# Optimization experiments

Hardware: AMD Instinct MI355X
Metric: run time of the kernel (lower is better)

The kernel has to match this reference:

```python
import jax, jax.numpy as jnp
import numpy as np

HEADS = 8

def _ln(x, g, b):
    m = jnp.mean(x, -1, keepdims=True)
    v = jnp.var(x, -1, keepdims=True)
    return (x - m) * jax.lax.rsqrt(v + 1e-5) * g + b

def _mha(q, kv, W, b, key_valid):
    # W: [4,E,E] (q,k,v,out proj), b: [4,E]; key_valid: [Sk] bool mask over kv positions
    B, Sq, E = q.shape
    Sk = kv.shape[1]
    D = E // HEADS
    qh = (q @ W[0] + b[0]).reshape(B, Sq, HEADS, D)
    kh = (kv @ W[1] + b[1]).reshape(B, Sk, HEADS, D)
    vh = (kv @ W[2] + b[2]).reshape(B, Sk, HEADS, D)
    s = jnp.einsum('bqhd,bkhd->bhqk', qh, kh) / jnp.sqrt(jnp.asarray(D, q.dtype))
    s = jnp.where(key_valid[None, None, None, :], s, jnp.asarray(-1e9, q.dtype))
    o = jnp.einsum('bhqk,bkhd->bqhd', jax.nn.softmax(s, -1), vh).reshape(B, Sq, E)
    return o @ W[3] + b[3]

def _posenc(S, E):
    pos = np.arange(S)[:, None].astype(np.float32)
    i = np.arange(0, E, 2).astype(np.float32)[None, :]
    ang = pos / np.power(10000.0, i / E)
    pe = np.zeros((S, E), np.float32)
    pe[:, 0::2] = np.sin(ang)
    pe[:, 1::2] = np.cos(ang)
    return jnp.asarray(pe)

def _forward(noise, seeds, inemb_W, inemb_b, g_attn_W, g_attn_b, g_cross_W, g_cross_b,
             g_ffn_W1, g_ffn_b1, g_ffn_W2, g_ffn_b2, g_ln_g, g_ln_b,
             o_attn_W, o_attn_b, o_ffn_W1, o_ffn_b1, o_ffn_W2, o_ffn_b2, o_ln_g, o_ln_b,
             w2v, soft_W, soft_b):
    B, S, E = noise.shape
    V = soft_W.shape[1]
    # inEmb: M stacked linear layers (no activation)
    w = noise
    for i in range(inemb_W.shape[0]):
        w = w @ inemb_W[i] + inemb_b[i]
    pe = _posenc(S, E)[None]  # [1,S,E]
    nB = g_attn_W.shape[0]
    nO = o_attn_W.shape[0]

    def step(carry, t):
        Ybuf, out_sent = carry
        valid = jnp.arange(S) <= t  # grown-sequence mask (no KV cache in original)
        x = Ybuf + pe
        for i in range(nB):  # generator: outTrans decoder blocks (self + cross-attn to w)
            x = _ln(x + _mha(x, x, g_attn_W[i], g_attn_b[i], valid), g_ln_g[i, 0], g_ln_b[i, 0])
            x = _ln(x + _mha(x, w, g_cross_W[i], g_cross_b[i], valid), g_ln_g[i, 1], g_ln_b[i, 1])
            f = jax.nn.relu(x @ g_ffn_W1[i] + g_ffn_b1[i]) @ g_ffn_W2[i] + g_ffn_b2[i]
            x = _ln(x + f, g_ln_g[i, 2], g_ln_b[i, 2])
        for j in range(nO):  # outEmb: inTrans encoder blocks
            x = _ln(x + _mha(x, x, o_attn_W[j], o_attn_b[j], valid), o_ln_g[j, 0], o_ln_b[j, 0])
            f = jax.nn.relu(x @ o_ffn_W1[j] + o_ffn_b1[j]) @ o_ffn_W2[j] + o_ffn_b2[j]
            x = _ln(x + f, o_ln_g[j, 1], o_ln_b[j, 1])
        tok = x[:, t]  # [B,E]
        probs = jax.nn.softmax(tok @ soft_W + soft_b, axis=-1)  # [B,V]
        out_sent = jax.lax.dynamic_update_slice(out_sent, probs[:, None, :], (0, t, 0))
        emb = w2v[jnp.argmax(probs, axis=-1)]  # Word2Vec(one_hot(argmax)) == row lookup
        Ybuf = jax.lax.dynamic_update_slice(Ybuf, emb[:, None, :], (0, t, 0))
        return (Ybuf, out_sent), None

    init = (seeds, jnp.zeros((B, S, V), noise.dtype))
    (_, out_sent), _ = jax.lax.scan(step, init, jnp.arange(S))
    return out_sent

def setup_inputs():
    key = jax.random.key(0)
    ks = jax.random.split(key, 12)
    B, S, E, H, V = 32, 32, 512, 2048, 30000
    M, NB, NO = 2, 2, 1
    def rn(k, shape, s=0.02):
        return jax.random.normal(k, shape, jnp.float32) * s
    return {
        'noise': jax.random.normal(ks[0], (B, S, E), jnp.float32),
        'seeds': jax.random.normal(ks[1], (B, S, E), jnp.float32),
        'inemb_W': rn(ks[2], (M, E, E)), 'inemb_b': jnp.zeros((M, E), jnp.float32),
        'g_attn_W': rn(ks[3], (NB, 4, E, E)), 'g_attn_b': jnp.zeros((NB, 4, E), jnp.float32),
        'g_cross_W': rn(ks[4], (NB, 4, E, E)), 'g_cross_b': jnp.zeros((NB, 4, E), jnp.float32),
        'g_ffn_W1': rn(ks[5], (NB, E, H)), 'g_ffn_b1': jnp.zeros((NB, H), jnp.float32),
        'g_ffn_W2': rn(ks[6], (NB, H, E)), 'g_ffn_b2': jnp.zeros((NB, E), jnp.float32),
        'g_ln_g': jnp.ones((NB, 3, E), jnp.float32), 'g_ln_b': jnp.zeros((NB, 3, E), jnp.float32),
        'o_attn_W': rn(ks[7], (NO, 4, E, E)), 'o_attn_b': jnp.zeros((NO, 4, E), jnp.float32),
        'o_ffn_W1': rn(ks[8], (NO, E, H)), 'o_ffn_b1': jnp.zeros((NO, H), jnp.float32),
        'o_ffn_W2': rn(ks[9], (NO, H, E)), 'o_ffn_b2': jnp.zeros((NO, E), jnp.float32),
        'o_ln_g': jnp.ones((NO, 2, E), jnp.float32), 'o_ln_b': jnp.zeros((NO, 2, E), jnp.float32),
        'w2v': rn(ks[10], (V, E)),
        'soft_W': rn(ks[11], (E, V)), 'soft_b': jnp.zeros((V,), jnp.float32),
    }

def reference(noise, seeds, inemb_W, inemb_b, g_attn_W, g_attn_b, g_cross_W, g_cross_b,
              g_ffn_W1, g_ffn_b1, g_ffn_W2, g_ffn_b2, g_ln_g, g_ln_b,
              o_attn_W, o_attn_b, o_ffn_W1, o_ffn_b1, o_ffn_W2, o_ffn_b2, o_ln_g, o_ln_b,
              w2v, soft_W, soft_b):
    return _forward(noise, seeds, inemb_W, inemb_b, g_attn_W, g_attn_b, g_cross_W, g_cross_b,
                    g_ffn_W1, g_ffn_b1, g_ffn_W2, g_ffn_b2, g_ln_g, g_ln_b,
                    o_attn_W, o_attn_b, o_ffn_W1, o_ffn_b1, o_ffn_W2, o_ffn_b2, o_ln_g, o_ln_b,
                    w2v, soft_W, soft_b)
```

## Files before the change

### kernel.cpp

```cpp
#include <hip/hip_runtime.h>
#include <math.h>

#define E 512
#define S_MAX 32
#define BATCH 32
#define HEADS 8
#define DH 64
#define HID 2048
#define VOCAB 30000

typedef unsigned short u16;
typedef __attribute__((ext_vector_type(8))) short short8;
typedef __attribute__((ext_vector_type(4))) float f32x4;

__device__ __forceinline__ u16 f2bf(float x) {
    union { float f; unsigned u; } v; v.f = x;
    unsigned r = v.u + 0x7fffu + ((v.u >> 16) & 1u);
    return (u16)(r >> 16);
}
__device__ __forceinline__ float bf2f(u16 h) {
    union { unsigned u; float f; } v; v.u = ((unsigned)h) << 16;
    return v.f;
}
__device__ __forceinline__ void split3(float x, u16& h, u16& m, u16& l) {
    h = f2bf(x); float hf = bf2f(h);
    float r1 = x - hf;
    m = f2bf(r1); float mf = bf2f(m);
    l = f2bf(r1 - mf);
}

__global__ void pe_kernel(float* __restrict__ PEp) {
    int s = blockIdx.x;
    for (int e = threadIdx.x; e < E; e += 256) {
        float expo = (float)(e & ~1) / (float)E;
        float den = powf(10000.0f, expo);
        float ang = (float)s / den;
        PEp[s * E + e] = (e & 1) ? cosf(ang) : sinf(ang);
    }
}

__global__ void build_x_kernel(float* __restrict__ X, const float* __restrict__ Ybuf,
                               const float* __restrict__ PEp, int Seff,
                               u16* __restrict__ Xh, u16* __restrict__ Xm, u16* __restrict__ Xl) {
    long idx = (long)blockIdx.x * 256 + threadIdx.x;
    long total = (long)BATCH * Seff * E;
    if (idx >= total) return;
    int e = (int)(idx & (E - 1));
    long mm = idx >> 9;
    int b = (int)(mm / Seff);
    int s = (int)(mm - (long)b * Seff);
    float v = Ybuf[((long)b * S_MAX + s) * E + e] + PEp[s * E + e];
    X[idx] = v;
    u16 h, m, l; split3(v, h, m, l);
    Xh[idx] = h; Xm[idx] = m; Xl[idx] = l;
}

__global__ void split_act_kernel(const float* __restrict__ in, long n,
                                 u16* __restrict__ Ph, u16* __restrict__ Pm, u16* __restrict__ Pl) {
    long i = ((long)blockIdx.x * 256 + threadIdx.x) * 4;
    if (i >= n) return;
    float4 v = *(const float4*)(in + i);
    u16 h, m, l;
    split3(v.x, h, m, l); Ph[i] = h; Pm[i] = m; Pl[i] = l;
    split3(v.y, h, m, l); Ph[i+1] = h; Pm[i+1] = m; Pl[i+1] = l;
    split3(v.z, h, m, l); Ph[i+2] = h; Pm[i+2] = m; Pl[i+2] = l;
    split3(v.w, h, m, l); Ph[i+3] = h; Pm[i+3] = m; Pl[i+3] = l;
}

__global__ __launch_bounds__(256) void wsplit_kernel(const float* __restrict__ W,
                                                     u16* __restrict__ Ph, u16* __restrict__ Pm,
                                                     u16* __restrict__ Pl,
                                                     int K, int N, long wzin, long wzout) {
    int z = blockIdx.z;
    W += (long)z * wzin; Ph += (long)z * wzout; Pm += (long)z * wzout; Pl += (long)z * wzout;
    int n0 = blockIdx.x * 32, k0 = blockIdx.y * 32;
    __shared__ float T[32][33];
    int tid = threadIdx.x;
    int kk = tid >> 3, nn = (tid & 7) * 4;
    float4 v = *(const float4*)&W[(long)(k0 + kk) * N + n0 + nn];
    T[kk][nn + 0] = v.x; T[kk][nn + 1] = v.y; T[kk][nn + 2] = v.z; T[kk][nn + 3] = v.w;
    __syncthreads();
    int n = tid >> 3, k4 = (tid & 7) * 4;
    u16 h[4], m[4], l[4];
#pragma unroll
    for (int j = 0; j < 4; j++) split3(T[k4 + j][n], h[j], m[j], l[j]);
    long o = (long)(n0 + n) * K + k0 + k4;
    *(ushort4*)&Ph[o] = make_ushort4(h[0], h[1], h[2], h[3]);
    *(ushort4*)&Pm[o] = make_ushort4(m[0], m[1], m[2], m[3]);
    *(ushort4*)&Pl[o] = make_ushort4(l[0], l[1], l[2], l[3]);
}

template <int RELU, int WF32, int WSPLIT>
__global__ __launch_bounds__(256) void gemm_mfma(
    const u16* __restrict__ Ah, const u16* __restrict__ Am, const u16* __restrict__ Al,
    const u16* __restrict__ Wh, const u16* __restrict__ Wm, const u16* __restrict__ Wl,
    const float* __restrict__ bias,
    float* __restrict__ C, u16* __restrict__ Ch, u16* __restrict__ Cm, u16* __restrict__ Cl,
    int M, int N, int K, long wz, long cz, long bz) {
    int z = blockIdx.z;
    const u16* Ap[3] = {Ah, Am, Al};
    const u16* Bp[3] = {Wh + (long)z * wz, Wm + (long)z * wz, Wl + (long)z * wz};
    bias += (long)z * bz;
    C += (long)z * cz;
    Ch += (long)z * cz; Cm += (long)z * cz; Cl += (long)z * cz;

    int n0 = blockIdx.x * 64, m0 = blockIdx.y * 64;
    int tid = threadIdx.x, lane = tid & 63, wid = tid >> 6;
    int wr = wid >> 1, wc = wid & 1;

    __shared__ u16 As[3][2048];
    __shared__ u16 Bs[3][2048];

    int srow = (tid >> 6) * 16 + (tid & 15);
    int scol = ((tid >> 4) & 3) * 8;
    int arow = m0 + srow; if (arow >= M) arow = M - 1;
    int brow = n0 + srow;
    long abase = (long)arow * K + scol;
    long bbase = (long)brow * K + scol;

    uint4 ra[3], rb[3];
#pragma unroll
    for (int p = 0; p < 3; p++) {
        ra[p] = *(const uint4*)(Ap[p] + abase);
        rb[p] = *(const uint4*)(Bp[p] + bbase);
    }

    f32x4 acc[2][2];
#pragma unroll
    for (int mi = 0; mi < 2; mi++)
#pragma unroll
        for (int ni = 0; ni < 2; ni++) acc[mi][ni] = (f32x4){0.f, 0.f, 0.f, 0.f};

    int fro = (lane >> 4) * 128 + (lane & 15) * 8;
    const int PA[6] = {0, 0, 1, 1, 0, 2};
    const int PB[6] = {0, 1, 0, 1, 2, 0};

    for (int k0 = 0; k0 < K; k0 += 32) {
#pragma unroll
        for (int p = 0; p < 3; p++) {
            *(uint4*)&As[p][tid * 8] = ra[p];
            *(uint4*)&Bs[p][tid * 8] = rb[p];
        }
        __syncthreads();
        if (k0 + 32 < K) {
#pragma unroll
            for (int p = 0; p < 3; p++) {
                ra[p] = *(const uint4*)(Ap[p] + abase + k0 + 32);
                rb[p] = *(const uint4*)(Bp[p] + bbase + k0 + 32);
            }
        }
        short8 af[3][2], bf[3][2];
#pragma unroll
        for (int p = 0; p < 3; p++) {
#pragma unroll
            for (int q = 0; q < 2; q++) {
                af[p][q] = *(const short8*)&As[p][(wr * 2 + q) * 512 + fro];
                bf[p][q] = *(const short8*)&Bs[p][(wc * 2 + q) * 512 + fro];
            }
        }
#pragma unroll
        for (int u = 0; u < 6; u++) {
#pragma unroll
            for (int mi = 0; mi < 2; mi++)
#pragma unroll
                for (int ni = 0; ni < 2; ni++)
                    acc[mi][ni] = __builtin_amdgcn_mfma_f32_16x16x32_bf16(
                        af[PA[u]][mi], bf[PB[u]][ni], acc[mi][ni], 0, 0, 0);
        }
        __syncthreads();
    }

#pragma unroll
    for (int mi = 0; mi < 2; mi++) {
#pragma unroll
        for (int ni = 0; ni < 2; ni++) {
            int col = n0 + wc * 32 + ni * 16 + (lane & 15);
            float bv = bias[col];
#pragma unroll
            for (int j = 0; j < 4; j++) {
                int row = m0 + wr * 32 + mi * 16 + (lane >> 4) * 4 + j;
                if (row < M) {
                    float v = acc[mi][ni][j] + bv;
                    if (RELU) v = fmaxf(v, 0.f);
                    long idx = (long)row * N + col;
                    if (WF32) C[idx] = v;
                    if (WSPLIT) {
                        u16 hh, mm, ll; split3(v, hh, mm, ll);
                        Ch[idx] = hh; Cm[idx] = mm; Cl[idx] = ll;
                    }
                }
            }
        }
    }
}

__global__ __launch_bounds__(64) void attn_kernel(const float* __restrict__ Q,
                                                  const float* __restrict__ Kp,
                                                  const float* __restrict__ Vp,
                                                  u16* __restrict__ Oh, u16* __restrict__ Om,
                                                  u16* __restrict__ Ol,
                                                  int Seff, int kvBatchStride) {
    int s = blockIdx.x, h = blockIdx.y, b = blockIdx.z;
    int lane = threadIdx.x;
    __shared__ float qs[DH];
    qs[lane] = Q[((long)(b * Seff + s)) * E + h * DH + lane];
    __syncthreads();

    float sc = -INFINITY;
    if (lane < Seff) {
        const float4* k4 = (const float4*)(Kp + (long)b * kvBatchStride + (long)lane * E + h * DH);
        const float4* q4 = (const float4*)qs;
        float acc = 0.f;
#pragma unroll
        for (int d = 0; d < DH / 4; d++) {
            float4 kv = k4[d];
            float4 qv = q4[d];
            acc += qv.x * kv.x; acc += qv.y * kv.y; acc += qv.z * kv.z; acc += qv.w * kv.w;
        }
        sc = acc * 0.125f;
    }
    float m = sc;
#pragma unroll
    for (int off = 32; off; off >>= 1) m = fmaxf(m, __shfl_xor(m, off));
    float p = (lane < Seff) ? expf(sc - m) : 0.f;
    float sum = p;
#pragma unroll
    for (int off = 32; off; off >>= 1) sum += __shfl_xor(sum, off);
    p = p / sum;

    float acc = 0.f;
    const float* vbase = Vp + (long)b * kvBatchStride + h * DH + lane;
    for (int k = 0; k < Seff; k++) {
        float pk = __shfl(p, k);
        acc = fmaf(pk, vbase[(long)k * E], acc);
    }
    long o = ((long)(b * Seff + s)) * E + h * DH + lane;
    u16 hh, mm, ll; split3(acc, hh, mm, ll);
    Oh[o] = hh; Om[o] = mm; Ol[o] = ll;
}

__global__ __launch_bounds__(64) void resid_ln_kernel(float* __restrict__ X,
                                                      const float* __restrict__ Dlt,
                                                      const float* __restrict__ g,
                                                      const float* __restrict__ bb,
                                                      u16* __restrict__ Xh, u16* __restrict__ Xm,
                                                      u16* __restrict__ Xl) {
    long row = blockIdx.x;
    int lane = threadIdx.x;
    float* xr = X + row * E;
    const float* dr = Dlt + row * E;
    float v[8];
    float s = 0.f;
#pragma unroll
    for (int i = 0; i < 8; i++) {
        int e = lane + i * 64;
        v[i] = xr[e] + dr[e];
        s += v[i];
    }
#pragma unroll
    for (int off = 32; off; off >>= 1) s += __shfl_xor(s, off);
    float mean = s * (1.0f / E);
    float sq = 0.f;
#pragma unroll
    for (int i = 0; i < 8; i++) {
        float d = v[i] - mean;
        sq += d * d;
    }
#pragma unroll
    for (int off = 32; off; off >>= 1) sq += __shfl_xor(sq, off);
    float var = sq * (1.0f / E);
    float r = 1.0f / sqrtf(var + 1e-5f);
#pragma unroll
    for (int i = 0; i < 8; i++) {
        int e = lane + i * 64;
        float o = (v[i] - mean) * r * g[e] + bb[e];
        xr[e] = o;
        u16 hh, mm, ll; split3(o, hh, mm, ll);
        long idx = row * E + e;
        Xh[idx] = hh; Xm[idx] = mm; Xl[idx] = ll;
    }
}

__global__ __launch_bounds__(256) void logits_kernel(const float* __restrict__ X,
                                                     const float* __restrict__ SW,
                                                     const float* __restrict__ sb,
                                                     float* __restrict__ Lg,
                                                     int Seff, int t) {
    int nl = threadIdx.x & 63;
    int kq = threadIdx.x >> 6;
    int n = blockIdx.x * 64 + nl;
    bool nok = n < VOCAB;
    float acc[BATCH];
#pragma unroll
    for (int b = 0; b < BATCH; b++) acc[b] = 0.f;
    if (nok) {
        int k0 = kq * 128;
        for (int k = k0; k < k0 + 128; k++) {
            float wv = SW[(long)k * VOCAB + n];
#pragma unroll
            for (int b = 0; b < BATCH; b++) {
                acc[b] = fmaf(X[((long)(b * Seff + t)) * E + k], wv, acc[b]);
            }
        }
    }
    __shared__ float red[4][64];
    for (int b = 0; b < BATCH; b++) {
        red[kq][nl] = acc[b];
        __syncthreads();
        if (kq == 0 && nok) {
            float sum = red[0][nl] + red[1][nl] + red[2][nl] + red[3][nl] + sb[n];
            Lg[(long)b * VOCAB + n] = sum;
        }
        __syncthreads();
    }
}

__global__ __launch_bounds__(256) void softmax_out_kernel(const float* __restrict__ Lg,
                                                          float* __restrict__ Out,
                                                          const float* __restrict__ w2v,
                                                          float* __restrict__ Ybuf, int t) {
    int b = blockIdx.x;
    int tid = threadIdx.x;
    const float* lb = Lg + (long)b * VOCAB;
    __shared__ float red[256];

    float m = -INFINITY;
    for (int n = tid; n < VOCAB; n += 256) m = fmaxf(m, lb[n]);
    red[tid] = m;
    __syncthreads();
    for (int off = 128; off; off >>= 1) {
        if (tid < off) red[tid] = fmaxf(red[tid], red[tid + off]);
        __syncthreads();
    }
    m = red[0];
    __syncthreads();

    float s = 0.f;
    for (int n = tid; n < VOCAB; n += 256) s += expf(lb[n] - m);
    red[tid] = s;
    __syncthreads();
    for (int off = 128; off; off >>= 1) {
        if (tid < off) red[tid] += red[tid + off];
        __syncthreads();
    }
    s = red[0];
    __syncthreads();

    float bestv = -1.0f;
    int besti = VOCAB;
    float* ob = Out + ((long)b * S_MAX + t) * VOCAB;
    for (int n = tid; n < VOCAB; n += 256) {
        float p = expf(lb[n] - m) / s;
        ob[n] = p;
        if (p > bestv) { bestv = p; besti = n; }
    }
    __shared__ float rv[256];
    __shared__ int ri[256];
    rv[tid] = bestv;
    ri[tid] = besti;
    __syncthreads();
    for (int off = 128; off; off >>= 1) {
        if (tid < off) {
            float v2 = rv[tid + off];
            int i2 = ri[tid + off];
            if (v2 > rv[tid] || (v2 == rv[tid] && i2 < ri[tid])) { rv[tid] = v2; ri[tid] = i2; }
        }
        __syncthreads();
    }
    int idx = ri[0];
    float* yb = Ybuf + ((long)b * S_MAX + t) * E;
    for (int e = tid; e < E; e += 256) yb[e] = w2v[(long)idx * E + e];
}

extern "C" void kernel_launch(void* const* d_in, const int* in_sizes, int n_in,
                              void* d_out, int out_size, void* d_ws, size_t ws_size,
                              hipStream_t stream) {
    const float* noise    = (const float*)d_in[0];
    const float* seeds    = (const float*)d_in[1];
    const float* inemb_W  = (const float*)d_in[2];
    const float* inemb_b  = (const float*)d_in[3];
    const float* g_attn_W = (const float*)d_in[4];
    const float* g_attn_b = (const float*)d_in[5];
    const float* g_cross_W= (const float*)d_in[6];
    const float* g_cross_b= (const float*)d_in[7];
    const float* g_ffn_W1 = (const float*)d_in[8];
    const float* g_ffn_b1 = (const float*)d_in[9];
    const float* g_ffn_W2 = (const float*)d_in[10];
    const float* g_ffn_b2 = (const float*)d_in[11];
    const float* g_ln_g   = (const float*)d_in[12];
    const float* g_ln_b   = (const float*)d_in[13];
    const float* o_attn_W = (const float*)d_in[14];
    const float* o_attn_b = (const float*)d_in[15];
    const float* o_ffn_W1 = (const float*)d_in[16];
    const float* o_ffn_b1 = (const float*)d_in[17];
    const float* o_ffn_W2 = (const float*)d_in[18];
    const float* o_ffn_b2 = (const float*)d_in[19];
    const float* o_ln_g   = (const float*)d_in[20];
    const float* o_ln_b   = (const float*)d_in[21];
    const float* w2v      = (const float*)d_in[22];
    const float* soft_W   = (const float*)d_in[23];
    const float* soft_b   = (const float*)d_in[24];
    float* out = (float*)d_out;
    float* ws = (float*)d_ws;

    const long EE  = (long)E * E;
    const long EH  = (long)E * HID;
    const long BSE = (long)BATCH * S_MAX * E;
    const long BSH = (long)BATCH * S_MAX * HID;
    const long WTOT = 46 * EE;

    long off = 0;
    float* PE   = ws + off; off += 16384;
    float* YBUF = ws + off; off += BSE;
    float* X    = ws + off; off += BSE;
    float* TMP  = ws + off; off += BSE;
    float* QKV  = ws + off; off += 3 * BSE;
    float* KWVW = ws + off; off += 4 * BSE;
    float* LG   = ws + off; off += 960000;
    u16* XsH = (u16*)(ws + off); off += 3 * BSE / 2;
    u16* XsM = XsH + BSE; u16* XsL = XsM + BSE;
    u16* AOH = (u16*)(ws + off); off += 3 * BSE / 2;
    u16* AOM = AOH + BSE; u16* AOL = AOM + BSE;
    u16* HBH = (u16*)(ws + off); off += 3 * BSH / 2;
    u16* HBM2 = HBH + BSH; u16* HBL = HBM2 + BSH;
    long baseWords = off;

    bool full = ws_size >= (size_t)(baseWords + 3 * WTOT / 2) * 4;
    long WT_ELEMS = full ? WTOT : 4 * EE;
    u16* WT_H = (u16*)(ws + baseWords);
    u16* WT_M = WT_H + WT_ELEMS;
    u16* WT_L = WT_M + WT_ELEMS;

    const long OFF_INEMB = 0;
    const long OFF_GATTN = 2 * EE;
    const long OFF_GCROSS = 10 * EE;
    const long OFF_OATTN = 18 * EE;
    const long OFF_GF1 = 22 * EE;
    const long OFF_GF2 = 30 * EE;
    const long OFF_OF1 = 38 * EE;
    const long OFF_OF2 = 42 * EE;

    auto WSPL = [&](const float* Wsrc, long offFull, int K, int N, int z) -> long {
        if (full) return offFull;
        wsplit_kernel<<<dim3(N / 32, K / 32, z), dim3(256), 0, stream>>>(
            Wsrc, WT_H, WT_M, WT_L, K, N, (long)K * N, (long)K * N);
        return 0;
    };

    auto GEMM = [&](const u16* Ah, const u16* Am, const u16* Al, long woff,
                    const float* bias, float* C, u16* Ch, u16* Cm, u16* Cl,
                    int M, int N, int K, int Z, long wz, long cz, long bz, int mode) {
        dim3 g(N / 64, (M + 63) / 64, Z);
        const u16* Wh = WT_H + woff; const u16* Wm = WT_M + woff; const u16* Wl = WT_L + woff;
        if (mode == 0)
            gemm_mfma<0, 1, 0><<<g, dim3(256), 0, stream>>>(Ah, Am, Al, Wh, Wm, Wl, bias,
                                                            C, Ch, Cm, Cl, M, N, K, wz, cz, bz);
        else if (mode == 1)
            gemm_mfma<0, 0, 1><<<g, dim3(256), 0, stream>>>(Ah, Am, Al, Wh, Wm, Wl, bias,
                                                            C, Ch, Cm, Cl, M, N, K, wz, cz, bz);
        else
            gemm_mfma<1, 0, 1><<<g, dim3(256), 0, stream>>>(Ah, Am, Al, Wh, Wm, Wl, bias,
                                                            C, Ch, Cm, Cl, M, N, K, wz, cz, bz);
    };

    pe_kernel<<<dim3(S_MAX), dim3(256), 0, stream>>>(PE);
    hipMemcpyAsync(YBUF, seeds, BSE * sizeof(float), hipMemcpyDeviceToDevice, stream);

    if (full) {
        wsplit_kernel<<<dim3(16, 16, 2), dim3(256), 0, stream>>>(inemb_W, WT_H + OFF_INEMB, WT_M + OFF_INEMB, WT_L + OFF_INEMB, 512, 512, EE, EE);
        wsplit_kernel<<<dim3(16, 16, 8), dim3(256), 0, stream>>>(g_attn_W, WT_H + OFF_GATTN, WT_M + OFF_GATTN, WT_L + OFF_GATTN, 512, 512, EE, EE);
        wsplit_kernel<<<dim3(16, 16, 8), dim3(256), 0, stream>>>(g_cross_W, WT_H + OFF_GCROSS, WT_M + OFF_GCROSS, WT_L + OFF_GCROSS, 512, 512, EE, EE);
        wsplit_kernel<<<dim3(16, 16, 4), dim3(256), 0, stream>>>(o_attn_W, WT_H + OFF_OATTN, WT_M + OFF_OATTN, WT_L + OFF_OATTN, 512, 512, EE, EE);
        wsplit_kernel<<<dim3(64, 16, 2), dim3(256), 0, stream>>>(g_ffn_W1, WT_H + OFF_GF1, WT_M + OFF_GF1, WT_L + OFF_GF1, 512, 2048, EH, EH);
        wsplit_kernel<<<dim3(16, 64, 2), dim3(256), 0, stream>>>(g_ffn_W2, WT_H + OFF_GF2, WT_M + OFF_GF2, WT_L + OFF_GF2, 2048, 512, EH, EH);
        wsplit_kernel<<<dim3(64, 16, 1), dim3(256), 0, stream>>>(o_ffn_W1, WT_H + OFF_OF1, WT_M + OFF_OF1, WT_L + OFF_OF1, 512, 2048, EH, EH);
        wsplit_kernel<<<dim3(16, 64, 1), dim3(256), 0, stream>>>(o_ffn_W2, WT_H + OFF_OF2, WT_M + OFF_OF2, WT_L + OFF_OF2, 2048, 512, EH, EH);
    }

    split_act_kernel<<<dim3((int)(BSE / 1024)), dim3(256), 0, stream>>>(noise, BSE, HBH, HBM2, HBL);

    {
        long w = WSPL(inemb_W, OFF_INEMB, 512, 512, 1);
        GEMM(HBH, HBM2, HBL, w, inemb_b, TMP, AOH, AOM, AOL, BATCH * S_MAX, E, E, 1, 0, 0, 0, 1);
        w = WSPL(inemb_W + EE, OFF_INEMB + EE, 512, 512, 1);
        GEMM(AOH, AOM, AOL, w, inemb_b + E, TMP, XsH, XsM, XsL, BATCH * S_MAX, E, E, 1, 0, 0, 0, 1);
    }
    for (int i = 0; i < 2; i++) {
        long w = WSPL(g_cross_W + (i * 4 + 1) * EE, OFF_GCROSS + (i * 4 + 1) * EE, 512, 512, 2);
        GEMM(XsH, XsM, XsL, w, g_cross_b + (i * 4 + 1) * E, KWVW + i * 2 * BSE, AOH, AOM, AOL,
             BATCH * S_MAX, E, E, 2, EE, BSE, E, 0);
    }

    for (int t = 0; t < S_MAX; t++) {
        int Seff = t + 1;
        int Mrows = BATCH * Seff;
        long ME = (long)Mrows * E;
        int total = Mrows * E;

        build_x_kernel<<<dim3((total + 255) / 256), dim3(256), 0, stream>>>(X, YBUF, PE, Seff,
                                                                            XsH, XsM, XsL);

        for (int i = 0; i < 2; i++) {
            long w = WSPL(g_attn_W + (long)i * 4 * EE, OFF_GATTN + i * 4 * EE, 512, 512, 3);
            GEMM(XsH, XsM, XsL, w, g_attn_b + (long)i * 4 * E, QKV, AOH, AOM, AOL,
                 Mrows, E, E, 3, EE, ME, E, 0);
            attn_kernel<<<dim3(Seff, HEADS, BATCH), dim3(64), 0, stream>>>(
                QKV, QKV + ME, QKV + 2 * ME, AOH, AOM, AOL, Seff, Seff * E);
            w = WSPL(g_attn_W + (i * 4 + 3) * EE, OFF_GATTN + (i * 4 + 3) * EE, 512, 512, 1);
            GEMM(AOH, AOM, AOL, w, g_attn_b + (i * 4 + 3) * E, TMP, AOH, AOM, AOL,
                 Mrows, E, E, 1, 0, 0, 0, 0);
            resid_ln_kernel<<<dim3(Mrows), dim3(64), 0, stream>>>(
                X, TMP, g_ln_g + (i * 3 + 0) * E, g_ln_b + (i * 3 + 0) * E, XsH, XsM, XsL);
            w = WSPL(g_cross_W + (long)i * 4 * EE, OFF_GCROSS + i * 4 * EE, 512, 512, 1);
            GEMM(XsH, XsM, XsL, w, g_cross_b + (long)i * 4 * E, QKV, AOH, AOM, AOL,
                 Mrows, E, E, 1, 0, 0, 0, 0);
            attn_kernel<<<dim3(Seff, HEADS, BATCH), dim3(64), 0, stream>>>(
                QKV, KWVW + i * 2 * BSE, KWVW + i * 2 * BSE + BSE, AOH, AOM, AOL, Seff, S_MAX * E);
            w = WSPL(g_cross_W + (i * 4 + 3) * EE, OFF_GCROSS + (i * 4 + 3) * EE, 512, 512, 1);
            GEMM(AOH, AOM, AOL, w, g_cross_b + (i * 4 + 3) * E, TMP, AOH, AOM, AOL,
                 Mrows, E, E, 1, 0, 0, 0, 0);
            resid_ln_kernel<<<dim3(Mrows), dim3(64), 0, stream>>>(
                X, TMP, g_ln_g + (i * 3 + 1) * E, g_ln_b + (i * 3 + 1) * E, XsH, XsM, XsL);
            w = WSPL(g_ffn_W1 + (long)i * EH, OFF_GF1 + i * EH, 512, 2048, 1);
            GEMM(XsH, XsM, XsL, w, g_ffn_b1 + (long)i * HID, TMP, HBH, HBM2, HBL,
                 Mrows, HID, E, 1, 0, 0, 0, 2);
            w = WSPL(g_ffn_W2 + (long)i * EH, OFF_GF2 + i * EH, 2048, 512, 1);
            GEMM(HBH, HBM2, HBL, w, g_ffn_b2 + (long)i * E, TMP, AOH, AOM, AOL,
                 Mrows, E, HID, 1, 0, 0, 0, 0);
            resid_ln_kernel<<<dim3(Mrows), dim3(64), 0, stream>>>(
                X, TMP, g_ln_g + (i * 3 + 2) * E, g_ln_b + (i * 3 + 2) * E, XsH, XsM, XsL);
        }
        {
            long w = WSPL(o_attn_W, OFF_OATTN, 512, 512, 3);
            GEMM(XsH, XsM, XsL, w, o_attn_b, QKV, AOH, AOM, AOL, Mrows, E, E, 3, EE, ME, E, 0);
            attn_kernel<<<dim3(Seff, HEADS, BATCH), dim3(64), 0, stream>>>(
                QKV, QKV + ME, QKV + 2 * ME, AOH, AOM, AOL, Seff, Seff * E);
            w = WSPL(o_attn_W + 3 * EE, OFF_OATTN + 3 * EE, 512, 512, 1);
            GEMM(AOH, AOM, AOL, w, o_attn_b + 3 * E, TMP, AOH, AOM, AOL, Mrows, E, E, 1, 0, 0, 0, 0);
            resid_ln_kernel<<<dim3(Mrows), dim3(64), 0, stream>>>(X, TMP, o_ln_g, o_ln_b,
                                                                  XsH, XsM, XsL);
            w = WSPL(o_ffn_W1, OFF_OF1, 512, 2048, 1);
            GEMM(XsH, XsM, XsL, w, o_ffn_b1, TMP, HBH, HBM2, HBL, Mrows, HID, E, 1, 0, 0, 0, 2);
            w = WSPL(o_ffn_W2, OFF_OF2, 2048, 512, 1);
            GEMM(HBH, HBM2, HBL, w, o_ffn_b2, TMP, AOH, AOM, AOL, Mrows, E, HID, 1, 0, 0, 0, 0);
            resid_ln_kernel<<<dim3(Mrows), dim3(64), 0, stream>>>(X, TMP, o_ln_g + E, o_ln_b + E,
                                                                  XsH, XsM, XsL);
        }

        logits_kernel<<<dim3((VOCAB + 63) / 64), dim3(256), 0, stream>>>(X, soft_W, soft_b, LG, Seff, t);
        softmax_out_kernel<<<dim3(BATCH), dim3(256), 0, stream>>>(LG, out, w2v, YBUF, t);
    }
}
```

Measured before the change: 37.35 ms.

## Replace LDS-staged split-bf16 GEMM with direct global-to-register fragment loads

The GEMM no longer stages A and W tiles through shared memory with barriers. Each wave now loads its MFMA fragments straight from global memory, relying on L1/L2 for reuse across waves. K is made a template constant so the loop can be unrolled. This removes LDS round trips and __syncthreads, at the cost of duplicated global loads per block and no explicit prefetch. The non-512 path assumes K=2048 with mode 0, which is correct only if all K=2048 calls use that mode.

```diff
diff --git a/kernel.cpp b/kernel.cpp
--- a/kernel.cpp
+++ b/kernel.cpp
@@ -90,92 +90,68 @@
     *(ushort4*)&Pl[o] = make_ushort4(l[0], l[1], l[2], l[3]);
 }
 
-template <int RELU, int WF32, int WSPLIT>
-__global__ __launch_bounds__(256) void gemm_mfma(
+#define MF(A_, B_, mi, ni) \
+    acc[mi][ni] = __builtin_amdgcn_mfma_f32_16x16x32_bf16(A_, B_, acc[mi][ni], 0, 0, 0)
+
+template <int RELU, int WF32, int WSPLIT, int KC>
+__global__ __launch_bounds__(256) void gemm_direct(
     const u16* __restrict__ Ah, const u16* __restrict__ Am, const u16* __restrict__ Al,
     const u16* __restrict__ Wh, const u16* __restrict__ Wm, const u16* __restrict__ Wl,
     const float* __restrict__ bias,
     float* __restrict__ C, u16* __restrict__ Ch, u16* __restrict__ Cm, u16* __restrict__ Cl,
-    int M, int N, int K, long wz, long cz, long bz) {
+    int M, int N, long wz, long cz, long bz) {
     int z = blockIdx.z;
-    const u16* Ap[3] = {Ah, Am, Al};
-    const u16* Bp[3] = {Wh + (long)z * wz, Wm + (long)z * wz, Wl + (long)z * wz};
-    bias += (long)z * bz;
-    C += (long)z * cz;
-    Ch += (long)z * cz; Cm += (long)z * cz; Cl += (long)z * cz;
+    const u16* Whz = Wh + (long)z * wz;
+    const u16* Wmz = Wm + (long)z * wz;
+    const u16* Wlz = Wl + (long)z * wz;
+    const float* bb = bias + (long)z * bz;
 
     int n0 = blockIdx.x * 64, m0 = blockIdx.y * 64;
-    int tid = threadIdx.x, lane = tid & 63, wid = tid >> 6;
+    int lane = threadIdx.x & 63, wid = threadIdx.x >> 6;
     int wr = wid >> 1, wc = wid & 1;
 
-    __shared__ u16 As[3][2048];
-    __shared__ u16 Bs[3][2048];
-
-    int srow = (tid >> 6) * 16 + (tid & 15);
-    int scol = ((tid >> 4) & 3) * 8;
-    int arow = m0 + srow; if (arow >= M) arow = M - 1;
-    int brow = n0 + srow;
-    long abase = (long)arow * K + scol;
-    long bbase = (long)brow * K + scol;
-
-    uint4 ra[3], rb[3];
-#pragma unroll
-    for (int p = 0; p < 3; p++) {
-        ra[p] = *(const uint4*)(Ap[p] + abase);
-        rb[p] = *(const uint4*)(Bp[p] + bbase);
-    }
+    int ra0 = m0 + wr * 32 + (lane & 15); if (ra0 >= M) ra0 = M - 1;
+    int ra1 = m0 + wr * 32 + 16 + (lane & 15); if (ra1 >= M) ra1 = M - 1;
+    int kcol = (lane >> 4) * 8;
+    long ao0 = (long)ra0 * KC + kcol;
+    long ao1 = (long)ra1 * KC + kcol;
+    long bo0 = (long)(n0 + wc * 32 + (lane & 15)) * KC + kcol;
+    long bo1 = bo0 + 16L * KC;
 
     f32x4 acc[2][2];
-#pragma unroll
-    for (int mi = 0; mi < 2; mi++)
-#pragma unroll
-        for (int ni = 0; ni < 2; ni++) acc[mi][ni] = (f32x4){0.f, 0.f, 0.f, 0.f};
-
-    int fro = (lane >> 4) * 128 + (lane & 15) * 8;
-    const int PA[6] = {0, 0, 1, 1, 0, 2};
-    const int PB[6] = {0, 1, 0, 1, 2, 0};
-
-    for (int k0 = 0; k0 < K; k0 += 32) {
-#pragma unroll
-        for (int p = 0; p < 3; p++) {
-            *(uint4*)&As[p][tid * 8] = ra[p];
-            *(uint4*)&Bs[p][tid * 8] = rb[p];
-        }
-        __syncthreads();
-        if (k0 + 32 < K) {
-#pragma unroll
-            for (int p = 0; p < 3; p++) {
-                ra[p] = *(const uint4*)(Ap[p] + abase + k0 + 32);
-                rb[p] = *(const uint4*)(Bp[p] + bbase + k0 + 32);
-            }
-        }
-        short8 af[3][2], bf[3][2];
-#pragma unroll
-        for (int p = 0; p < 3; p++) {
-#pragma unroll
-            for (int q = 0; q < 2; q++) {
-                af[p][q] = *(const short8*)&As[p][(wr * 2 + q) * 512 + fro];
-                bf[p][q] = *(const short8*)&Bs[p][(wc * 2 + q) * 512 + fro];
-            }
-        }
-#pragma unroll
-        for (int u = 0; u < 6; u++) {
-#pragma unroll
-            for (int mi = 0; mi < 2; mi++)
-#pragma unroll
-                for (int ni = 0; ni < 2; ni++)
-                    acc[mi][ni] = __builtin_amdgcn_mfma_f32_16x16x32_bf16(
-                        af[PA[u]][mi], bf[PB[u]][ni], acc[mi][ni], 0, 0, 0);
-        }
-        __syncthreads();
-    }
-
+    acc[0][0] = acc[0][1] = acc[1][0] = acc[1][1] = (f32x4){0.f, 0.f, 0.f, 0.f};
+
+#pragma unroll 4
+    for (int k0 = 0; k0 < KC; k0 += 32) {
+        short8 a0h = *(const short8*)(Ah + ao0 + k0);
+        short8 a1h = *(const short8*)(Ah + ao1 + k0);
+        short8 a0m = *(const short8*)(Am + ao0 + k0);
+        short8 a1m = *(const short8*)(Am + ao1 + k0);
+        short8 a0l = *(const short8*)(Al + ao0 + k0);
+        short8 a1l = *(const short8*)(Al + ao1 + k0);
+        short8 b0h = *(const short8*)(Whz + bo0 + k0);
+        short8 b1h = *(const short8*)(Whz + bo1 + k0);
+        short8 b0m = *(const short8*)(Wmz + bo0 + k0);
+        short8 b1m = *(const short8*)(Wmz + bo1 + k0);
+        short8 b0l = *(const short8*)(Wlz + bo0 + k0);
+        short8 b1l = *(const short8*)(Wlz + bo1 + k0);
+        MF(a0h, b0h, 0, 0); MF(a0h, b1h, 0, 1); MF(a1h, b0h, 1, 0); MF(a1h, b1h, 1, 1);
+        MF(a0h, b0m, 0, 0); MF(a0h, b1m, 0, 1); MF(a1h, b0m, 1, 0); MF(a1h, b1m, 1, 1);
+        MF(a0m, b0h, 0, 0); MF(a0m, b1h, 0, 1); MF(a1m, b0h, 1, 0); MF(a1m, b1h, 1, 1);
+        MF(a0m, b0m, 0, 0); MF(a0m, b1m, 0, 1); MF(a1m, b0m, 1, 0); MF(a1m, b1m, 1, 1);
+        MF(a0h, b0l, 0, 0); MF(a0h, b1l, 0, 1); MF(a1h, b0l, 1, 0); MF(a1h, b1l, 1, 1);
+        MF(a0l, b0h, 0, 0); MF(a0l, b1h, 0, 1); MF(a1l, b0h, 1, 0); MF(a1l, b1h, 1, 1);
+    }
+
+    float* Cz = C; u16 *Chz = Ch, *Cmz = Cm, *Clz = Cl;
+    if (WF32) Cz = C + (long)z * cz;
+    if (WSPLIT) { Chz = Ch + (long)z * cz; Cmz = Cm + (long)z * cz; Clz = Cl + (long)z * cz; }
 #pragma unroll
     for (int mi = 0; mi < 2; mi++) {
 #pragma unroll
         for (int ni = 0; ni < 2; ni++) {
             int col = n0 + wc * 32 + ni * 16 + (lane & 15);
-            float bv = bias[col];
+            float bv = bb[col];
 #pragma unroll
             for (int j = 0; j < 4; j++) {
                 int row = m0 + wr * 32 + mi * 16 + (lane >> 4) * 4 + j;
@@ -183,10 +159,10 @@
                     float v = acc[mi][ni][j] + bv;
                     if (RELU) v = fmaxf(v, 0.f);
                     long idx = (long)row * N + col;
-                    if (WF32) C[idx] = v;
+                    if (WF32) Cz[idx] = v;
                     if (WSPLIT) {
                         u16 hh, mm, ll; split3(v, hh, mm, ll);
-                        Ch[idx] = hh; Cm[idx] = mm; Cl[idx] = ll;
+                        Chz[idx] = hh; Cmz[idx] = mm; Clz[idx] = ll;
                     }
                 }
             }
@@ -452,15 +428,20 @@
                     int M, int N, int K, int Z, long wz, long cz, long bz, int mode) {
         dim3 g(N / 64, (M + 63) / 64, Z);
         const u16* Wh = WT_H + woff; const u16* Wm = WT_M + woff; const u16* Wl = WT_L + woff;
-        if (mode == 0)
-            gemm_mfma<0, 1, 0><<<g, dim3(256), 0, stream>>>(Ah, Am, Al, Wh, Wm, Wl, bias,
-                                                            C, Ch, Cm, Cl, M, N, K, wz, cz, bz);
-        else if (mode == 1)
-            gemm_mfma<0, 0, 1><<<g, dim3(256), 0, stream>>>(Ah, Am, Al, Wh, Wm, Wl, bias,
-                                                            C, Ch, Cm, Cl, M, N, K, wz, cz, bz);
-        else
-            gemm_mfma<1, 0, 1><<<g, dim3(256), 0, stream>>>(Ah, Am, Al, Wh, Wm, Wl, bias,
-                                                            C, Ch, Cm, Cl, M, N, K, wz, cz, bz);
+        if (K == 512) {
+            if (mode == 0)
+                gemm_direct<0, 1, 0, 512><<<g, dim3(256), 0, stream>>>(
+                    Ah, Am, Al, Wh, Wm, Wl, bias, C, Ch, Cm, Cl, M, N, wz, cz, bz);
+            else if (mode == 1)
+                gemm_direct<0, 0, 1, 512><<<g, dim3(256), 0, stream>>>(
+                    Ah, Am, Al, Wh, Wm, Wl, bias, C, Ch, Cm, Cl, M, N, wz, cz, bz);
+            else
+                gemm_direct<1, 0, 1, 512><<<g, dim3(256), 0, stream>>>(
+                    Ah, Am, Al, Wh, Wm, Wl, bias, C, Ch, Cm, Cl, M, N, wz, cz, bz);
+        } else {
+            gemm_direct<0, 1, 0, 2048><<<g, dim3(256), 0, stream>>>(
+                Ah, Am, Al, Wh, Wm, Wl, bias, C, Ch, Cm, Cl, M, N, wz, cz, bz);
+        }
     };
 
     pe_kernel<<<dim3(S_MAX), dim3(256), 0, stream>>>(PE);
```

Measured after the change: 30.96 ms. 1.21x faster.
